# Kernel optimization log

Measured on AMD Instinct MI355X. Metric: run time of the kernel, lower is better.

Reference implementation:

```python
import jax, jax.numpy as jnp
import numpy as np

B, N, K, CIN, COUT = 2, 8192, 16, 64, 64


def setup_inputs() -> dict:
    key = jax.random.key(0)
    ks = jax.random.split(key, 12)
    w = lambda k, shape: jax.random.normal(k, shape, jnp.float32) * 0.02
    return dict(
        pos=jax.random.normal(ks[0], (B, N, 3), jnp.float32),
        features=jax.random.normal(ks[1], (B, N, CIN), jnp.float32),
        emb_w=w(ks[2], (CIN, COUT)), emb_b=jnp.zeros((COUT,), jnp.float32),
        wq=w(ks[3], (COUT, COUT)), wk=w(ks[4], (COUT, COUT)), wv=w(ks[5], (COUT, COUT)),
        pe_w1=w(ks[6], (3, COUT)), pe_b1=jnp.zeros((COUT,), jnp.float32),
        pe_w2=w(ks[7], (COUT, COUT)), pe_b2=jnp.zeros((COUT,), jnp.float32),
        at_w1=w(ks[8], (COUT, COUT)), at_b1=jnp.zeros((COUT,), jnp.float32),
        at_w2=w(ks[9], (COUT, COUT)), at_b2=jnp.zeros((COUT,), jnp.float32),
        out_w=w(ks[10], (COUT, CIN)), out_b=jnp.zeros((CIN,), jnp.float32),
    )


def _gather(x, idx):
    # x: [B, N, C], idx: [B, N, K] -> [B, N, K, C]
    return jax.vmap(lambda xb, ib: xb[ib])(x, idx)


def reference(pos, features, emb_w, emb_b, wq, wk, wv,
              pe_w1, pe_b1, pe_w2, pe_b2,
              at_w1, at_b1, at_w2, at_b2, out_w, out_b):
    # KNN: squared pairwise distances, take k smallest (includes self)
    sq = jnp.sum(pos * pos, axis=-1)                                  # [B, N]
    d2 = sq[:, :, None] + sq[:, None, :] - 2.0 * jnp.einsum('bnd,bmd->bnm', pos, pos)
    _, knn_idx = jax.lax.top_k(-d2, K)                                # [B, N, K]

    # recenter_groups: neighbor positions relative to query point
    grouped_pos = _gather(pos, knn_idx) - pos[:, :, None, :]          # [B, N, K, 3]

    x = features @ emb_w + emb_b                                      # [B, N, COUT]
    q = x @ wq                                                        # [B, N, COUT]
    k = _gather(x @ wk, knn_idx)                                      # [B, N, K, COUT]
    v = _gather(x @ wv, knn_idx)                                      # [B, N, K, COUT]

    # mlp_posenc: Linear(3,C) -> ReLU -> Linear(C,C)
    posenc = jax.nn.relu(grouped_pos @ pe_w1 + pe_b1) @ pe_w2 + pe_b2  # [B, N, K, COUT]

    # mlp_attn on (q - k + posenc), softmax over neighbor axis (dim=-2)
    h = q[:, :, None, :] - k + posenc
    attn = jax.nn.relu(h @ at_w1 + at_b1) @ at_w2 + at_b2
    attn = jax.nn.softmax(attn / np.float32(np.sqrt(COUT)), axis=-2)

    result = jnp.einsum('bmnf,bmnf->bmf', attn, v + posenc)           # [B, N, COUT]
    return result @ out_w + out_b + features                          # [B, N, CIN]
```

## Files before the change

### kernel.cpp

```cpp
#include <hip/hip_runtime.h>
#include <hip/hip_bf16.h>

#define BB 2
#define NN 8192
#define SPL 16
#define CAND (NN/SPL)
#define NPTS (BB*NN)

#define POS4_OFF 0u
#define PART_OFF 65536u
#define IDX_OFF  4259840u
#define WT_OFF   4521984u
#define QB_OFF   4530176u
#define KVB_OFF  5578752u

typedef __attribute__((ext_vector_type(8))) short bf16x8;
typedef __attribute__((ext_vector_type(4))) float f32x4;

__device__ __forceinline__ unsigned umn(unsigned a, unsigned b) {
#if __has_builtin(__builtin_elementwise_min)
  return __builtin_elementwise_min(a, b);
#else
  return a < b ? a : b;
#endif
}
__device__ __forceinline__ unsigned umx(unsigned a, unsigned b) {
#if __has_builtin(__builtin_elementwise_max)
  return __builtin_elementwise_max(a, b);
#else
  return a < b ? b : a;
#endif
}

__device__ inline unsigned short f2bf(float x) {
  __hip_bfloat16 b = __float2bfloat16(x);
  return *(unsigned short*)&b;
}

#define HCOL(c, j) ((((((c) >> 3) + (j)) & 7) << 3) | ((c) & 7))

#define SORTB(CC, JBASE)                                                    \
  do {                                                                      \
    unsigned b[16];                                                         \
    _Pragma("unroll")                                                       \
    for (int i = 0; i < 16; i++) {                                          \
      const float cx = CC[(3 * i) >> 2][(3 * i) & 3];                       \
      const float cy = CC[(3 * i + 1) >> 2][(3 * i + 1) & 3];               \
      const float cz = CC[(3 * i + 2) >> 2][(3 * i + 2) & 3];               \
      float dx = cx - qx, dy = cy - qy, dz = cz - qz;                       \
      float d2 = fmaf(dx, dx, fmaf(dy, dy, dz * dz));                       \
      b[i] = (__float_as_uint(d2) & 0xFFFFE000u) |                          \
             (jb + (unsigned)((JBASE) + i));                                \
    }                                                                       \
    _Pragma("unroll")                                                       \
    for (int cc2 = 0; cc2 < 63; cc2++) {                                    \
      const int x = OE[cc2][0], y = OE[cc2][1];                             \
      unsigned lo = umn(b[x], b[y]);                                        \
      unsigned hi = umx(b[x], b[y]);                                        \
      b[x] = hi; b[y] = lo;                                                 \
    }                                                                       \
    _Pragma("unroll")                                                       \
    for (int i = 0; i < 16; i++) m[i] = umn(m[i], b[i]);                    \
    _Pragma("unroll")                                                       \
    for (int d = 8; d; d >>= 1) {                                           \
      _Pragma("unroll")                                                     \
      for (int i = 0; i < 16; i++) {                                        \
        if ((i & d) == 0) {                                                 \
          const int l = i | d;                                              \
          unsigned lo = umn(m[i], m[l]);                                    \
          unsigned hi = umx(m[i], m[l]);                                    \
          m[i] = lo; m[l] = hi;                                             \
        }                                                                   \
      }                                                                     \
    }                                                                       \
  } while (0)

__global__ __launch_bounds__(256) void mega1(
    const float* __restrict__ pos, const float* __restrict__ feat,
    const float* __restrict__ emb_w, const float* __restrict__ emb_b,
    const float* __restrict__ wq, const float* __restrict__ wk,
    const float* __restrict__ wv,
    const float* __restrict__ pe_w2, const float* __restrict__ at_w1,
    const float* __restrict__ at_w2, const float* __restrict__ out_w,
    float* __restrict__ ws)
{
  __shared__ __align__(16) float smem[6144];
  const int tid = threadIdx.x;
  const int bx = blockIdx.x;
  float* pos4 = ws + POS4_OFF;
  unsigned* part = (unsigned*)ws + PART_OFF;
  float* qg = ws + QB_OFF;
  unsigned* kvp = (unsigned*)ws + KVB_OFF;

  if (bx < 1024) {
    constexpr int OE[63][2] = {
      {0,1},{2,3},{4,5},{6,7},{8,9},{10,11},{12,13},{14,15},
      {0,2},{1,3},{4,6},{5,7},{8,10},{9,11},{12,14},{13,15},
      {1,2},{5,6},{9,10},{13,14},
      {0,4},{1,5},{2,6},{3,7},{8,12},{9,13},{10,14},{11,15},
      {2,4},{3,5},{10,12},{11,13},
      {1,2},{3,4},{5,6},{9,10},{11,12},{13,14},
      {0,8},{1,9},{2,10},{3,11},{4,12},{5,13},{6,14},{7,15},
      {4,8},{5,9},{6,10},{7,11},
      {2,4},{3,5},{6,8},{7,9},{10,12},{11,13},
      {1,2},{3,4},{5,6},{7,8},{9,10},{11,12},{13,14}
    };
    const int g = (bx & 63) * 256 + tid;
    const int s = bx >> 6;
    const int bu = __builtin_amdgcn_readfirstlane(g >> 13);
    const float qx = pos[g * 3 + 0], qy = pos[g * 3 + 1], qz = pos[g * 3 + 2];
    const unsigned jb = (unsigned)(s * CAND);
    {
      const f32x4* segp = (const f32x4*)(pos + (bu * NN + s * CAND) * 3);
      f32x4* cl4w = (f32x4*)smem;
      for (int i = tid; i < 384; i += 256) cl4w[i] = segp[i];
    }
    __syncthreads();
    const f32x4* cl4 = (const f32x4*)smem;
    unsigned m[16];
#pragma unroll
    for (int i = 0; i < 16; i++) m[i] = 0xFFFFFFFFu;
    f32x4 ca[12], cb[12];
#pragma unroll
    for (int i = 0; i < 12; i++) ca[i] = cl4[i];
    for (int j0 = 0; j0 < CAND; j0 += 32) {
      const int b1 = ((j0 >> 4) + 1) * 12;
#pragma unroll
      for (int i = 0; i < 12; i++) cb[i] = cl4[b1 + i];
      SORTB(ca, j0);
      const int b2 = ((j0 + 32 < CAND) ? ((j0 >> 4) + 2) : ((j0 >> 4) + 1)) * 12;
#pragma unroll
      for (int i = 0; i < 12; i++) ca[i] = cl4[b2 + i];
      SORTB(cb, j0 + 16);
    }
#pragma unroll
    for (int i = 0; i < 16; i++)
      part[(unsigned)(s * 16 + i) * NPTS + (unsigned)g] = m[i];
  } else if (bx < 1536) {
    float* wl = smem;
    float* xl = smem + 4096;
    const int vb = bx - 1024;
    const int col = tid & 63;
    const int rg = tid >> 6;
    const int row0 = vb * 32 + rg * 8;
    const int rowu = __builtin_amdgcn_readfirstlane(row0);
    if (tid < 32) {
      const int p = vb * 32 + tid;
      float x = pos[p * 3 + 0], y = pos[p * 3 + 1], z = pos[p * 3 + 2];
      float4 v = {x, y, z, 0.f};
      ((float4*)pos4)[p] = v;
    }
    for (int i = tid; i < 4096; i += 256) wl[i] = emb_w[i];
    __syncthreads();
    {
      float acc[8];
      float bias = emb_b[col];
#pragma unroll
      for (int r = 0; r < 8; r++) acc[r] = bias;
      for (int c = 0; c < 64; c++) {
        float w = wl[c * 64 + col];
        const float* fp = feat + rowu * 64 + c;
#pragma unroll
        for (int r = 0; r < 8; r++) acc[r] = fmaf(fp[r * 64], w, acc[r]);
      }
#pragma unroll
      for (int r = 0; r < 8; r++) xl[(rg * 8 + r) * 64 + col] = acc[r];
    }
    __syncthreads();
    for (int i = tid; i < 4096; i += 256) wl[i] = wq[i];
    __syncthreads();
    {
      float aq[8];
#pragma unroll
      for (int r = 0; r < 8; r++) aq[r] = 0.f;
      for (int c = 0; c < 64; c++) {
        float w = wl[c * 64 + col];
#pragma unroll
        for (int r = 0; r < 8; r++)
          aq[r] = fmaf(xl[(rg * 8 + r) * 64 + c], w, aq[r]);
      }
#pragma unroll
      for (int r = 0; r < 8; r++) qg[(row0 + r) * 64 + col] = aq[r];
    }
    __syncthreads();
    for (int i = tid; i < 4096; i += 256) wl[i] = wk[i];
    __syncthreads();
    float ak[8];
    {
#pragma unroll
      for (int r = 0; r < 8; r++) ak[r] = 0.f;
      for (int c = 0; c < 64; c++) {
        float w = wl[c * 64 + col];
#pragma unroll
        for (int r = 0; r < 8; r++)
          ak[r] = fmaf(xl[(rg * 8 + r) * 64 + c], w, ak[r]);
      }
    }
    __syncthreads();
    for (int i = tid; i < 4096; i += 256) wl[i] = wv[i];
    __syncthreads();
    {
      float av[8];
#pragma unroll
      for (int r = 0; r < 8; r++) av[r] = 0.f;
      for (int c = 0; c < 64; c++) {
        float w = wl[c * 64 + col];
#pragma unroll
        for (int r = 0; r < 8; r++)
          av[r] = fmaf(xl[(rg * 8 + r) * 64 + c], w, av[r]);
      }
#pragma unroll
      for (int r = 0; r < 8; r++)
        kvp[(row0 + r) * 64 + col] =
            ((unsigned)f2bf(av[r]) << 16) | (unsigned)f2bf(ak[r]);
    }
  } else {
    const int t = (bx - 1536) * 256 + tid;
    const float* s;
    switch (t >> 12) {
      case 0: s = pe_w2; break;
      case 1: s = at_w1; break;
      case 2: s = at_w2; break;
      default: s = out_w; break;
    }
    const int idx = t & 4095, f = idx >> 6, c = idx & 63;
    ((unsigned short*)(ws + WT_OFF))[t] = f2bf(s[c * 64 + f]);
  }
}

__global__ __launch_bounds__(256) void s3_merge(const float* __restrict__ ws_ro,
                                                int* __restrict__ knn_idx)
{
  const unsigned* part = (const unsigned*)ws_ro + PART_OFF;
  const int g = blockIdx.x * 256 + threadIdx.x;
  unsigned run[16];
#pragma unroll
  for (int i = 0; i < 16; i++) run[i] = part[i * NPTS + g];
#pragma unroll
  for (int l = 1; l < SPL; l++) {
#pragma unroll
    for (int i = 0; i < 16; i++)
      run[i] = umn(run[i], part[(l * 16 + 15 - i) * NPTS + g]);
#pragma unroll
    for (int d = 8; d; d >>= 1) {
#pragma unroll
      for (int i = 0; i < 16; i++) {
        if ((i & d) == 0) {
          const int l2 = i | d;
          unsigned lo = umn(run[i], run[l2]);
          unsigned hi = umx(run[i], run[l2]);
          run[i] = lo; run[l2] = hi;
        }
      }
    }
  }
  const int base = (g >> 13) * NN;
  int outv[16];
#pragma unroll
  for (int i = 0; i < 16; i++) outv[i] = base + (int)(run[i] & 0x1FFFu);
  int4* o = (int4*)(knn_idx + g * 16);
  o[0] = make_int4(outv[0], outv[1], outv[2], outv[3]);
  o[1] = make_int4(outv[4], outv[5], outv[6], outv[7]);
  o[2] = make_int4(outv[8], outv[9], outv[10], outv[11]);
  o[3] = make_int4(outv[12], outv[13], outv[14], outv[15]);
}

__device__ inline void mv(const unsigned short* hm, const bf16x8 B[4][2],
                          const float bias[4], int ln, int s0, int s1,
                          f32x4 acc[4])
{
  bf16x8 a0 = *(const bf16x8*)(hm + ln * 64 + s0);
  bf16x8 a1 = *(const bf16x8*)(hm + ln * 64 + s1);
#pragma unroll
  for (int t = 0; t < 4; t++) {
    f32x4 a = {bias[t], bias[t], bias[t], bias[t]};
    a = __builtin_amdgcn_mfma_f32_16x16x32_bf16(a0, B[t][0], a, 0, 0, 0);
    a = __builtin_amdgcn_mfma_f32_16x16x32_bf16(a1, B[t][1], a, 0, 0, 0);
    acc[t] = a;
  }
}

__global__ __launch_bounds__(256, 2) void s4_attn(
    const float* __restrict__ ws_ro, const float* __restrict__ feat,
    const float* __restrict__ pe_w1, const float* __restrict__ pe_b1,
    const float* __restrict__ pe_b2, const float* __restrict__ at_b1,
    const float* __restrict__ at_b2, const float* __restrict__ out_b,
    const int* __restrict__ knn, float* __restrict__ out)
{
  __shared__ unsigned short hma[4][1024];
  __shared__ unsigned short resm[1024];
  const float* pos4 = ws_ro + POS4_OFF;
  const float* qg = ws_ro + QB_OFF;
  const unsigned* kvp = (const unsigned*)ws_ro + KVB_OFF;
  const unsigned short* wt = (const unsigned short*)(ws_ro + WT_OFF);

  const int tid = threadIdx.x;
  const int wid = tid >> 6, lane = tid & 63;
  const int ln = lane & 15, quad = lane >> 4;
  unsigned short* hm = hma[wid];
  const int s0 = ((quad + ln) & 7) << 3;
  const int s1 = ((4 + quad + ln) & 7) << 3;

  bf16x8 Bf[3][4][2];
#pragma unroll
  for (int m = 0; m < 3; m++)
#pragma unroll
    for (int t = 0; t < 4; t++)
#pragma unroll
      for (int ks = 0; ks < 2; ks++)
        Bf[m][t][ks] = *(const bf16x8*)(wt + m * 4096 + (t * 16 + ln) * 64 +
                                        ks * 32 + quad * 8);
  bf16x8 bo[2];
#pragma unroll
  for (int ks = 0; ks < 2; ks++)
    bo[ks] = *(const bf16x8*)(wt + 3 * 4096 + (wid * 16 + ln) * 64 +
                              ks * 32 + quad * 8);

  float pw10 = pe_w1[lane], pw11 = pe_w1[64 + lane], pw12 = pe_w1[128 + lane];
  float pb1 = pe_b1[lane];
  float bpe[4], ba1[4], ba2[4];
#pragma unroll
  for (int t = 0; t < 4; t++) {
    bpe[t] = pe_b2[t * 16 + ln];
    ba1[t] = at_b1[t * 16 + ln];
    ba2[t] = at_b2[t * 16 + ln];
  }
  const float4* pp4 = (const float4*)pos4;

  const int p0 = blockIdx.x * 16 + wid * 4;
  const int ps0 = __builtin_amdgcn_readfirstlane(p0);
  int4 cur[4];
  {
    const int4* ip4 = (const int4*)(knn + ps0 * 16);
#pragma unroll
    for (int u = 0; u < 4; u++) cur[u] = ip4[u];
  }

  for (int pp = 0; pp < 4; pp++) {
    const int p = p0 + pp;
    const int ps = __builtin_amdgcn_readfirstlane(p);
    int jj[16];
#pragma unroll
    for (int u = 0; u < 4; u++) {
      jj[u*4+0] = cur[u].x; jj[u*4+1] = cur[u].y;
      jj[u*4+2] = cur[u].z; jj[u*4+3] = cur[u].w;
    }
    int4 nxt[4];
    {
      const int pn = (pp < 3) ? (ps + 1) : ps;
      const int4* np4 = (const int4*)(knn + pn * 16);
#pragma unroll
      for (int u = 0; u < 4; u++) nxt[u] = np4[u];
    }
    unsigned kvw[4][4];
#pragma unroll
    for (int r = 0; r < 4; r++) {
      const unsigned* kp = kvp + jj[quad * 4 + r] * 64 + ln;
#pragma unroll
      for (int t = 0; t < 4; t++) kvw[r][t] = kp[t * 16];
    }
    float qv[4];
#pragma unroll
    for (int t = 0; t < 4; t++) qv[t] = qg[p * 64 + t * 16 + ln];

    const float4 mp = pp4[ps];
#pragma unroll
    for (int j = 0; j < 16; j++) {
      const float4 np = pp4[jj[j]];
      float h1 = fmaf(np.z - mp.z, pw12,
                 fmaf(np.y - mp.y, pw11,
                 fmaf(np.x - mp.x, pw10, pb1)));
      hm[j * 64 + HCOL(lane, j)] = f2bf(fmaxf(h1, 0.f));
    }
    f32x4 accp[4];
    mv(hm, Bf[0], bpe, ln, s0, s1, accp);
    float vpe[4][4];
#pragma unroll
    for (int r = 0; r < 4; r++) {
      const int j = quad * 4 + r;
#pragma unroll
      for (int t = 0; t < 4; t++) {
        const unsigned w = kvw[r][t];
        float kf = __uint_as_float(w << 16);
        float vf = __uint_as_float(w & 0xFFFF0000u);
        float pe = accp[t][r];
        vpe[t][r] = vf + pe;
        hm[j * 64 + HCOL(t * 16 + ln, j)] = f2bf(qv[t] - kf + pe);
      }
    }
    f32x4 acch[4];
    mv(hm, Bf[1], ba1, ln, s0, s1, acch);
#pragma unroll
    for (int t = 0; t < 4; t++)
#pragma unroll
      for (int r = 0; r < 4; r++) {
        const int j = quad * 4 + r;
        hm[j * 64 + HCOL(t * 16 + ln, j)] = f2bf(fmaxf(acch[t][r], 0.f));
      }
    f32x4 lg[4];
    mv(hm, Bf[2], ba2, ln, s0, s1, lg);
    const int pb = wid * 4 + pp;
#pragma unroll
    for (int t = 0; t < 4; t++) {
      float e0 = __expf(lg[t][0] * 0.125f);
      float e1 = __expf(lg[t][1] * 0.125f);
      float e2 = __expf(lg[t][2] * 0.125f);
      float e3 = __expf(lg[t][3] * 0.125f);
      float ss = (e0 + e1) + (e2 + e3);
      float dt = fmaf(e3, vpe[t][3], fmaf(e2, vpe[t][2],
                 fmaf(e1, vpe[t][1], e0 * vpe[t][0])));
      ss += __shfl_xor(ss, 16); ss += __shfl_xor(ss, 32);
      dt += __shfl_xor(dt, 16); dt += __shfl_xor(dt, 32);
      float res = dt / ss;
      if (quad == 0) resm[pb * 64 + HCOL(t * 16 + ln, pb)] = f2bf(res);
    }
#pragma unroll
    for (int u = 0; u < 4; u++) cur[u] = nxt[u];
  }
  __syncthreads();
  {
    const int nt = wid;
    float ob = out_b[nt * 16 + ln];
    f32x4 acc = {ob, ob, ob, ob};
#pragma unroll
    for (int ks = 0; ks < 2; ks++) {
      bf16x8 a = *(const bf16x8*)(resm + ln * 64 +
                                  (((ks * 4 + quad + ln) & 7) << 3));
      acc = __builtin_amdgcn_mfma_f32_16x16x32_bf16(a, bo[ks], acc, 0, 0, 0);
    }
#pragma unroll
    for (int r = 0; r < 4; r++) {
      const int pt = blockIdx.x * 16 + quad * 4 + r;
      const int f = nt * 16 + ln;
      out[pt * 64 + f] = acc[r] + feat[pt * 64 + f];
    }
  }
}

extern "C" void kernel_launch(void* const* d_in, const int* in_sizes, int n_in,
                              void* d_out, int out_size, void* d_ws, size_t ws_size,
                              hipStream_t stream)
{
  (void)in_sizes; (void)n_in; (void)out_size; (void)ws_size;
  const float* pos   = (const float*)d_in[0];
  const float* feat  = (const float*)d_in[1];
  const float* emb_w = (const float*)d_in[2];
  const float* emb_b = (const float*)d_in[3];
  const float* wq    = (const float*)d_in[4];
  const float* wk    = (const float*)d_in[5];
  const float* wv    = (const float*)d_in[6];
  const float* pe_w1 = (const float*)d_in[7];
  const float* pe_b1 = (const float*)d_in[8];
  const float* pe_w2 = (const float*)d_in[9];
  const float* pe_b2 = (const float*)d_in[10];
  const float* at_w1 = (const float*)d_in[11];
  const float* at_b1 = (const float*)d_in[12];
  const float* at_w2 = (const float*)d_in[13];
  const float* at_b2 = (const float*)d_in[14];
  const float* out_w = (const float*)d_in[15];
  const float* out_b = (const float*)d_in[16];
  float* ws = (float*)d_ws;

  mega1<<<1600, 256, 0, stream>>>(pos, feat, emb_w, emb_b, wq, wk, wv,
                                  pe_w2, at_w1, at_w2, out_w, ws);
  s3_merge<<<64, 256, 0, stream>>>(ws, (int*)ws + IDX_OFF);
  s4_attn<<<NPTS / 16, 256, 0, stream>>>(ws, feat, pe_w1, pe_b1, pe_b2,
      at_b1, at_b2, out_b, (int*)ws + IDX_OFF, (float*)d_out);
}
```

Before: 226.8 us.

## Fuse KNN partial merge into attention kernel via shared-memory transpose

Removes the separate merge kernel and performs the 16-way partial top-k merge inside the attention kernel: each block loads its 16 points' partial lists (re-laid out in mega1 so they are contiguous per thread) into LDS, one lane per point merges them, and the resulting indices stay in LDS. This drops a kernel launch and the global round trip of knn indices. In exchange, only 16 lanes per block do the serial merge while the rest wait at a barrier, and the LDS footprint grows, which could reduce occupancy.

```diff
diff --git a/kernel.cpp b/kernel.cpp
--- a/kernel.cpp
+++ b/kernel.cpp
@@ -9,7 +9,6 @@
 
 #define POS4_OFF 0u
 #define PART_OFF 65536u
-#define IDX_OFF  4259840u
 #define WT_OFF   4521984u
 #define QB_OFF   4530176u
 #define KVB_OFF  5578752u
@@ -133,9 +132,12 @@
       for (int i = 0; i < 12; i++) ca[i] = cl4[b2 + i];
       SORTB(cb, j0 + 16);
     }
-#pragma unroll
-    for (int i = 0; i < 16; i++)
-      part[(unsigned)(s * 16 + i) * NPTS + (unsigned)g] = m[i];
+    {
+      const unsigned gg = (unsigned)(bx & 63);
+#pragma unroll
+      for (int i = 0; i < 16; i++)
+        part[gg * 65536u + (unsigned)(s * 16 + i) * 256u + (unsigned)tid] = m[i];
+    }
   } else if (bx < 1536) {
     float* wl = smem;
     float* xl = smem + 4096;
@@ -228,43 +230,6 @@
   }
 }
 
-__global__ __launch_bounds__(256) void s3_merge(const float* __restrict__ ws_ro,
-                                                int* __restrict__ knn_idx)
-{
-  const unsigned* part = (const unsigned*)ws_ro + PART_OFF;
-  const int g = blockIdx.x * 256 + threadIdx.x;
-  unsigned run[16];
-#pragma unroll
-  for (int i = 0; i < 16; i++) run[i] = part[i * NPTS + g];
-#pragma unroll
-  for (int l = 1; l < SPL; l++) {
-#pragma unroll
-    for (int i = 0; i < 16; i++)
-      run[i] = umn(run[i], part[(l * 16 + 15 - i) * NPTS + g]);
-#pragma unroll
-    for (int d = 8; d; d >>= 1) {
-#pragma unroll
-      for (int i = 0; i < 16; i++) {
-        if ((i & d) == 0) {
-          const int l2 = i | d;
-          unsigned lo = umn(run[i], run[l2]);
-          unsigned hi = umx(run[i], run[l2]);
-          run[i] = lo; run[l2] = hi;
-        }
-      }
-    }
-  }
-  const int base = (g >> 13) * NN;
-  int outv[16];
-#pragma unroll
-  for (int i = 0; i < 16; i++) outv[i] = base + (int)(run[i] & 0x1FFFu);
-  int4* o = (int4*)(knn_idx + g * 16);
-  o[0] = make_int4(outv[0], outv[1], outv[2], outv[3]);
-  o[1] = make_int4(outv[4], outv[5], outv[6], outv[7]);
-  o[2] = make_int4(outv[8], outv[9], outv[10], outv[11]);
-  o[3] = make_int4(outv[12], outv[13], outv[14], outv[15]);
-}
-
 __device__ inline void mv(const unsigned short* hm, const bf16x8 B[4][2],
                           const float bias[4], int ln, int s0, int s1,
                           f32x4 acc[4])
@@ -285,10 +250,10 @@
     const float* __restrict__ pe_w1, const float* __restrict__ pe_b1,
     const float* __restrict__ pe_b2, const float* __restrict__ at_b1,
     const float* __restrict__ at_b2, const float* __restrict__ out_b,
-    const int* __restrict__ knn, float* __restrict__ out)
+    float* __restrict__ out)
 {
-  __shared__ unsigned short hma[4][1024];
-  __shared__ unsigned short resm[1024];
+  __shared__ __align__(16) unsigned char smbuf[16448];
+  __shared__ __align__(16) int knn_l[256];
   const float* pos4 = ws_ro + POS4_OFF;
   const float* qg = ws_ro + QB_OFF;
   const unsigned* kvp = (const unsigned*)ws_ro + KVB_OFF;
@@ -297,7 +262,58 @@
   const int tid = threadIdx.x;
   const int wid = tid >> 6, lane = tid & 63;
   const int ln = lane & 15, quad = lane >> 4;
-  unsigned short* hm = hma[wid];
+  const int bx = blockIdx.x;
+
+  {
+    unsigned* plds = (unsigned*)smbuf;
+    const unsigned* part = (const unsigned*)ws_ro + PART_OFF;
+    const unsigned gg = (unsigned)(bx >> 4);
+    const unsigned gi0 = (unsigned)((bx & 15) * 16);
+    const unsigned* prow = part + gg * 65536u + (unsigned)tid * 256u + gi0;
+    uint4 r0 = ((const uint4*)prow)[0];
+    uint4 r1 = ((const uint4*)prow)[1];
+    uint4 r2 = ((const uint4*)prow)[2];
+    uint4 r3 = ((const uint4*)prow)[3];
+    unsigned vals[16] = {r0.x, r0.y, r0.z, r0.w, r1.x, r1.y, r1.z, r1.w,
+                         r2.x, r2.y, r2.z, r2.w, r3.x, r3.y, r3.z, r3.w};
+#pragma unroll
+    for (int j = 0; j < 16; j++) plds[j * 257 + tid] = vals[j];
+    __syncthreads();
+    if ((lane & 15) == 0) {
+      const int pj = wid * 4 + (lane >> 4);
+      const unsigned* pl = plds + pj * 257;
+      unsigned run[16];
+#pragma unroll
+      for (int i = 0; i < 16; i++) run[i] = pl[i];
+#pragma unroll
+      for (int l = 1; l < SPL; l++) {
+#pragma unroll
+        for (int i = 0; i < 16; i++)
+          run[i] = umn(run[i], pl[l * 16 + 15 - i]);
+#pragma unroll
+        for (int d = 8; d; d >>= 1) {
+#pragma unroll
+          for (int i = 0; i < 16; i++) {
+            if ((i & d) == 0) {
+              const int l2 = i | d;
+              unsigned lo = umn(run[i], run[l2]);
+              unsigned hi = umx(run[i], run[l2]);
+              run[i] = lo; run[l2] = hi;
+            }
+          }
+        }
+      }
+      const int p = bx * 16 + pj;
+      const int base = (p >> 13) * NN;
+#pragma unroll
+      for (int i = 0; i < 16; i++)
+        knn_l[pj * 16 + i] = base + (int)(run[i] & 0x1FFFu);
+    }
+    __syncthreads();
+  }
+
+  unsigned short* hm = (unsigned short*)smbuf + wid * 1024;
+  unsigned short* resm = (unsigned short*)smbuf + 4096;
   const int s0 = ((quad + ln) & 7) << 3;
   const int s1 = ((4 + quad + ln) & 7) << 3;
 
@@ -327,11 +343,10 @@
   }
   const float4* pp4 = (const float4*)pos4;
 
-  const int p0 = blockIdx.x * 16 + wid * 4;
-  const int ps0 = __builtin_amdgcn_readfirstlane(p0);
+  const int p0 = bx * 16 + wid * 4;
   int4 cur[4];
   {
-    const int4* ip4 = (const int4*)(knn + ps0 * 16);
+    const int4* ip4 = (const int4*)(knn_l + (wid * 4) * 16);
 #pragma unroll
     for (int u = 0; u < 4; u++) cur[u] = ip4[u];
   }
@@ -347,8 +362,8 @@
     }
     int4 nxt[4];
     {
-      const int pn = (pp < 3) ? (ps + 1) : ps;
-      const int4* np4 = (const int4*)(knn + pn * 16);
+      const int qn = (pp < 3) ? (wid * 4 + pp + 1) : (wid * 4 + pp);
+      const int4* np4 = (const int4*)(knn_l + qn * 16);
 #pragma unroll
       for (int u = 0; u < 4; u++) nxt[u] = np4[u];
     }
@@ -430,7 +445,7 @@
     }
 #pragma unroll
     for (int r = 0; r < 4; r++) {
-      const int pt = blockIdx.x * 16 + quad * 4 + r;
+      const int pt = bx * 16 + quad * 4 + r;
       const int f = nt * 16 + ln;
       out[pt * 64 + f] = acc[r] + feat[pt * 64 + f];
     }
@@ -463,7 +478,6 @@
 
   mega1<<<1600, 256, 0, stream>>>(pos, feat, emb_w, emb_b, wq, wk, wv,
                                   pe_w2, at_w1, at_w2, out_w, ws);
-  s3_merge<<<64, 256, 0, stream>>>(ws, (int*)ws + IDX_OFF);
   s4_attn<<<NPTS / 16, 256, 0, stream>>>(ws, feat, pe_w1, pe_b1, pe_b2,
-      at_b1, at_b2, out_b, (int*)ws + IDX_OFF, (float*)d_out);
-}
+      at_b1, at_b2, out_b, (float*)d_out);
+}
```

New measurement: 248.5 us. +9.6%, slower.
